# Performance work log

Hardware: AMD Instinct MI355X
Metric: run time of the kernel (lower is better)

Reference implementation:

```python
import jax, jax.numpy as jnp
import numpy as np
from jax import lax

B, T, N, C_IN = 1024, 10, 113, 4
E = N * 16
INV_STD = float(1.0 / np.sqrt(1.0 + 1e-5))  # eval-mode BatchNorm, running_mean=0, running_var=1
_DN = ('NHWC', 'HWIO', 'NHWC')  # (B,T,N,C) treated as NHWC, conv kernel (kt,1,Cin,Cout)


def _tconv(x, w, b):
    # x: (B,t,N,Cin), w: (3,1,Cin,Cout) -> (B,t-2,N,Cout); == Conv2d(Cin,Cout,(1,3)) in the torch layout
    return lax.conv_general_dilated(x, w, (1, 1), 'VALID', dimension_numbers=_DN) + b


def _gated_tcn(x, wp, bp, wq, bq, wr, br):
    # TemporalConv: relu(P * sigmoid(Q) + R)
    return jax.nn.relu(_tconv(x, wp, bp) * jax.nn.sigmoid(_tconv(x, wq, bq)) + _tconv(x, wr, br))


def _stconv(x, wp1, bp1, wq1, bq1, wr1, br1, cw, cb, wp2, bp2, wq2, bq2, wr2, br2, g, beta):
    h = _gated_tcn(x, wp1, bp1, wq1, bq1, wr1, br1)
    # ChebConv with K=1: only the identity term T_0 = x -> per-node linear (edge_index unused)
    h = jax.nn.relu(h @ cw + cb)
    h = _gated_tcn(h, wp2, bp2, wq2, bq2, wr2, br2)
    # BatchNorm2d over the node dim, eval mode (mean 0, var 1)
    return h * INV_STD * g[None, None, :, None] + beta[None, None, :, None]


def setup_inputs() -> dict:
    key = jax.random.key(0)
    ks = iter(jax.random.split(key, 48))

    def nrm(shape, s=0.1):
        return jax.random.normal(next(ks), shape, jnp.float32) * s

    d = {'x': nrm((B, T, N, C_IN), 1.0),
         'edge_index': jax.random.randint(next(ks), (2, E), 0, N)}
    # STConv block 1: in=4, hidden=32, out=64, kernel_size=3, K=1
    d['a_wp'] = nrm((3, 1, 4, 32)); d['a_bp'] = nrm((32,))
    d['a_wq'] = nrm((3, 1, 4, 32)); d['a_bq'] = nrm((32,))
    d['a_wr'] = nrm((3, 1, 4, 32)); d['a_br'] = nrm((32,))
    d['a_cw'] = nrm((32, 32));      d['a_cb'] = nrm((32,))
    d['a_wp2'] = nrm((3, 1, 32, 64)); d['a_bp2'] = nrm((64,))
    d['a_wq2'] = nrm((3, 1, 32, 64)); d['a_bq2'] = nrm((64,))
    d['a_wr2'] = nrm((3, 1, 32, 64)); d['a_br2'] = nrm((64,))
    d['a_g'] = jnp.ones((N,), jnp.float32); d['a_beta'] = jnp.zeros((N,), jnp.float32)
    # STConv block 2: in=64, hidden=32, out=16, kernel_size=3, K=1
    d['b_wp'] = nrm((3, 1, 64, 32)); d['b_bp'] = nrm((32,))
    d['b_wq'] = nrm((3, 1, 64, 32)); d['b_bq'] = nrm((32,))
    d['b_wr'] = nrm((3, 1, 64, 32)); d['b_br'] = nrm((32,))
    d['b_cw'] = nrm((32, 32));       d['b_cb'] = nrm((32,))
    d['b_wp2'] = nrm((3, 1, 32, 16)); d['b_bp2'] = nrm((16,))
    d['b_wq2'] = nrm((3, 1, 32, 16)); d['b_bq2'] = nrm((16,))
    d['b_wr2'] = nrm((3, 1, 32, 16)); d['b_br2'] = nrm((16,))
    d['b_g'] = jnp.ones((N,), jnp.float32); d['b_beta'] = jnp.zeros((N,), jnp.float32)
    # 113 per-node MLPs Linear(32,64)->ReLU->Linear(64,3), stacked as batched matmuls
    d['mlp_w1'] = nrm((N, 64, 32)); d['mlp_b1'] = nrm((N, 64))
    d['mlp_w2'] = nrm((N, 3, 64));  d['mlp_b2'] = nrm((N, 3))
    return d


def reference(x, edge_index, a_wp, a_bp, a_wq, a_bq, a_wr, a_br, a_cw, a_cb,
              a_wp2, a_bp2, a_wq2, a_bq2, a_wr2, a_br2, a_g, a_beta,
              b_wp, b_bp, b_wq, b_bq, b_wr, b_br, b_cw, b_cb,
              b_wp2, b_bp2, b_wq2, b_bq2, b_wr2, b_br2, b_g, b_beta,
              mlp_w1, mlp_b1, mlp_w2, mlp_b2):
    # dropout is identity in eval mode
    h = jax.nn.relu(_stconv(x, a_wp, a_bp, a_wq, a_bq, a_wr, a_br, a_cw, a_cb,
                            a_wp2, a_bp2, a_wq2, a_bq2, a_wr2, a_br2, a_g, a_beta))
    h = jax.nn.relu(_stconv(h, b_wp, b_bp, b_wq, b_bq, b_wr, b_br, b_cw, b_cb,
                            b_wp2, b_bp2, b_wq2, b_bq2, b_wr2, b_br2, b_g, b_beta))
    # h: (B, 2, N, 16); torch flatten(x[:,:,k,:], start_dim=1) interleaves (t, c) -> (B, N, 32)
    feat = jnp.transpose(h, (0, 2, 1, 3)).reshape(h.shape[0], N, 32)
    # all 113 tiny MLPs fused into two batched matmuls
    hid = jax.nn.relu(jnp.einsum('bnf,nhf->bnh', feat, mlp_w1) + mlp_b1)
    return jnp.einsum('bnh,noh->bno', hid, mlp_w2) + mlp_b2  # (B, 113, 3)
```

## Files before the change

### kernel.cpp

```cpp
#include <hip/hip_runtime.h>
#include <hip/hip_bf16.h>
#include <math.h>


namespace {

constexpr int NT = 512;
constexpr int NP = 32;
constexpr float INV_STD = 0.9999950000374997f;

typedef __attribute__((ext_vector_type(8))) short bf16x8;
typedef __attribute__((ext_vector_type(4))) float f32x4;

constexpr int OFF_CHEB_A = 0;
constexpr int OFF_CHEB_B = 1024;
constexpr int OFF_A2     = 2048;
constexpr int OFF_B1     = 20480;
constexpr int OFF_B2     = 38912;
constexpr int OFF_S1B    = 43520;
constexpr int OFF_W1     = 46592;
constexpr int OFF_W2     = 278016;

__device__ __forceinline__ unsigned short f2bf(float f){
  unsigned int u = __float_as_uint(f);
  u += 0x7fffu + ((u >> 16) & 1u);
  return (unsigned short)(u >> 16);
}
__device__ __forceinline__ unsigned short f2bf_fast(float f){
  return __bfloat16_as_ushort(__float2bfloat16(f));
}
__device__ __forceinline__ f32x4 bcast(float v){ f32x4 r; r[0]=v; r[1]=v; r[2]=v; r[3]=v; return r; }

struct Params {
  const float *x;
  const float *awp,*abp,*awq,*abq,*awr,*abr,*acw,*acb;
  const float *awp2,*abp2,*awq2,*abq2,*awr2,*abr2,*ag,*abeta;
  const float *bwp,*bbp,*bwq,*bbq,*bwr,*bbr,*bcw,*bcb;
  const float *bwp2,*bbp2,*bwq2,*bbq2,*bwr2,*bbr2,*bg,*bbeta;
  const float *w1,*b1,*w2,*b2;
  float *out;
};

__global__ void stgcn_prep(const Params p, unsigned short* __restrict__ W)
{
  int e = blockIdx.x*256 + threadIdx.x;
  if (e < 2048){
    const float* src = (e < 1024) ? p.acw : p.bcw;
    const int j = e & 1023, co = j >> 5, k = j & 31;
    W[e] = f2bf(src[k*32 + co]);
    return;
  }
  e -= 2048;
  if (e < 18432){
    const int mat = e / 6144, j = e % 6144, co = j / 96, k = j % 96;
    const float* src = mat==0 ? p.awp2 : (mat==1 ? p.awq2 : p.awr2);
    W[OFF_A2 + e] = f2bf(src[k*64 + co]);
    return;
  }
  e -= 18432;
  if (e < 18432){
    const int mat = e / 6144, j = e % 6144, co = j / 192, k = j % 192;
    const float* src = mat==0 ? p.bwp : (mat==1 ? p.bwq : p.bwr);
    W[OFF_B1 + e] = f2bf(src[k*32 + co]);
    return;
  }
  e -= 18432;
  if (e < 4608){
    const int mat = e / 1536, j = e % 1536, co = j / 96, k = j % 96;
    const float* src = mat==0 ? p.bwp2 : (mat==1 ? p.bwq2 : p.bwr2);
    W[OFF_B2 + e] = f2bf(src[k*16 + co]);
    return;
  }
  e -= 4608;
  if (e < 3072){
    const int mat = e / 1024, j = e % 1024, co = j >> 5, k = j & 31;
    const int tt = k >> 3, ci = k & 7;
    const float* src = mat==0 ? p.awp : (mat==1 ? p.awq : p.awr);
    W[OFF_S1B + e] = (ci < 4 && tt < 3) ? f2bf(src[(tt*4+ci)*32 + co])
                                        : (unsigned short)0;
    return;
  }
  e -= 3072;
  if (e < 231424){ W[OFF_W1 + e] = f2bf(p.w1[e]); return; }
  e -= 231424;
  if (e < 21696){ W[OFF_W2 + e] = f2bf(p.w2[e]); }
}

template<int TOUT, int CIN, int COUT, int NK, int RSTI, int PSTI, int RSTO, int PSTO,
         int KP, int EPI, int MJOBS, int MSTEP, bool RELOADB>
__device__ __forceinline__ void mfma_stage(const unsigned short* __restrict__ aB,
    const unsigned short* __restrict__ gW, unsigned short* __restrict__ oB,
    const float* __restrict__ gb0, const float* __restrict__ gb1,
    const float* __restrict__ gb2,
    const int Mtile0, const int Ntile, const int lm, const int lk,
    const float bnsc, const float bnbt)
{
  const unsigned short* wbase = gW + (Ntile*16 + lm)*KP + lk*8;
  const int colbase = Ntile*16 + lk*4;
  bf16x8 wp[NK], wq[NK], wr[NK];
  if constexpr (!RELOADB){
    #pragma unroll
    for (int ks = 0; ks < NK; ++ks){
      wp[ks] = *reinterpret_cast<const bf16x8*>(wbase + ks*32);
      if constexpr (EPI >= 1){
        wq[ks] = *reinterpret_cast<const bf16x8*>(wbase +   COUT*KP + ks*32);
        wr[ks] = *reinterpret_cast<const bf16x8*>(wbase + 2*COUT*KP + ks*32);
      }
    }
  }
  const f32x4 b0v = *reinterpret_cast<const f32x4*>(gb0 + colbase);
  f32x4 b1v, b2v;
  if constexpr (EPI >= 1){
    b1v = *reinterpret_cast<const f32x4*>(gb1 + colbase);
    b2v = *reinterpret_cast<const f32x4*>(gb2 + colbase);
  }

  #pragma unroll 1
  for (int j = 0; j < MJOBS; ++j){
    const int m  = (Mtile0 + j*MSTEP)*16 + lm;
    const int pr = m / TOUT;
    const int t  = m - pr*TOUT;
    f32x4 aP = b0v, aQ, aR;
    if constexpr (EPI >= 1){ aQ = b1v; aR = b2v; }
    #pragma unroll
    for (int ks = 0; ks < NK; ++ks){
      bf16x8 fp, fq, fr;
      if constexpr (RELOADB){
        fp = *reinterpret_cast<const bf16x8*>(wbase + ks*32);
        if constexpr (EPI >= 1){
          fq = *reinterpret_cast<const bf16x8*>(wbase +   COUT*KP + ks*32);
          fr = *reinterpret_cast<const bf16x8*>(wbase + 2*COUT*KP + ks*32);
        }
      } else {
        fp = wp[ks];
        if constexpr (EPI >= 1){ fq = wq[ks]; fr = wr[ks]; }
      }
      int elem;
      if constexpr (CIN == 32) elem = pr*PSTI + (t + ks)*RSTI + lk*8;
      else                     elem = pr*PSTI + (t + (ks>>1))*RSTI + (ks&1)*32 + lk*8;
      const bf16x8 a = *reinterpret_cast<const bf16x8*>(aB + elem);
      aP = __builtin_amdgcn_mfma_f32_16x16x32_bf16(fp, a, aP, 0, 0, 0);
      if constexpr (EPI >= 1){
        aQ = __builtin_amdgcn_mfma_f32_16x16x32_bf16(fq, a, aQ, 0, 0, 0);
        aR = __builtin_amdgcn_mfma_f32_16x16x32_bf16(fr, a, aR, 0, 0, 0);
      }
    }
    ushort4 pk;
    unsigned short pv[4];
    #pragma unroll
    for (int r = 0; r < 4; ++r){
      float v;
      if constexpr (EPI == 0) v = fmaxf(aP[r], 0.f);
      else {
        const float sig = 1.f/(1.f + __expf(-aQ[r]));
        v = fmaxf(fmaf(aP[r], sig, aR[r]), 0.f);
        if constexpr (EPI == 2) v = fmaxf(fmaf(v, bnsc, bnbt), 0.f);
      }
      pv[r] = f2bf_fast(v);
    }
    pk.x = pv[0]; pk.y = pv[1]; pk.z = pv[2]; pk.w = pv[3];
    *reinterpret_cast<ushort4*>(oB + pr*PSTO + t*RSTO + colbase) = pk;
  }
}

__device__ __forceinline__ void mfma_stage4(const unsigned short* __restrict__ aB,
    const unsigned short* __restrict__ gW, unsigned short* __restrict__ oB,
    const float* __restrict__ gb0, const float* __restrict__ gb1,
    const float* __restrict__ gb2,
    const int Mtile0, const int Ntile, const int lm, const int lk)
{
  const unsigned short* wbase = gW + (Ntile*16 + lm)*192 + lk*8;
  const int colbase = Ntile*16 + lk*4;
  f32x4 aP[2], aQ[2], aR[2];
  {
    const f32x4 b0v = *reinterpret_cast<const f32x4*>(gb0 + colbase);
    const f32x4 b1v = *reinterpret_cast<const f32x4*>(gb1 + colbase);
    const f32x4 b2v = *reinterpret_cast<const f32x4*>(gb2 + colbase);
    #pragma unroll
    for (int j=0;j<2;++j){ aP[j]=b0v; aQ[j]=b1v; aR[j]=b2v; }
  }
  #pragma unroll 1
  for (int kb = 0; kb < 2; ++kb){
    bf16x8 wp[3], wq[3], wr[3];
    #pragma unroll
    for (int s = 0; s < 3; ++s){
      const int ks = kb*3 + s;
      wp[s] = *reinterpret_cast<const bf16x8*>(wbase +         ks*32);
      wq[s] = *reinterpret_cast<const bf16x8*>(wbase +  6144 + ks*32);
      wr[s] = *reinterpret_cast<const bf16x8*>(wbase + 12288 + ks*32);
    }
    #pragma unroll
    for (int j = 0; j < 2; ++j){
      const int m  = (Mtile0 + j*4)*16 + lm;
      const int pr = m >> 2, t = m & 3;
      #pragma unroll
      for (int s = 0; s < 3; ++s){
        const int ks = kb*3 + s;
        const int elem = pr*432 + (t + (ks>>1))*72 + (ks&1)*32 + lk*8;
        const bf16x8 a = *reinterpret_cast<const bf16x8*>(aB + elem);
        aP[j] = __builtin_amdgcn_mfma_f32_16x16x32_bf16(wp[s], a, aP[j], 0,0,0);
        aQ[j] = __builtin_amdgcn_mfma_f32_16x16x32_bf16(wq[s], a, aQ[j], 0,0,0);
        aR[j] = __builtin_amdgcn_mfma_f32_16x16x32_bf16(wr[s], a, aR[j], 0,0,0);
      }
    }
  }
  #pragma unroll
  for (int j = 0; j < 2; ++j){
    const int m  = (Mtile0 + j*4)*16 + lm;
    const int pr = m >> 2, t = m & 3;
    ushort4 pk;
    unsigned short pv[4];
    #pragma unroll
    for (int r = 0; r < 4; ++r){
      const float sig = 1.f/(1.f + __expf(-aQ[j][r]));
      pv[r] = f2bf_fast(fmaxf(fmaf(aP[j][r], sig, aR[j][r]), 0.f));
    }
    pk.x = pv[0]; pk.y = pv[1]; pk.z = pv[2]; pk.w = pv[3];
    *reinterpret_cast<ushort4*>(oB + pr*160 + t*40 + colbase) = pk;
  }
}

__global__ __launch_bounds__(NT, 6) void stgcn_main(const Params p,
    const unsigned short* __restrict__ W)
{
  __shared__ __align__(16) unsigned short smem[24064];
  unsigned short* const bufA = smem;
  unsigned short* const bufB = smem + 13824;
  unsigned short* const sxb  = bufB;

  const int tid = threadIdx.x;
  const int l   = tid & 63;
  const int wid = tid >> 6;
  const int lm  = l & 15;
  const int lk  = l >> 4;
  const int n   = blockIdx.x >> 5;
  const int b0  = (blockIdx.x & 31) * NP;

  for (int i = tid; i < NP*22; i += NT){
    const int pr = i / 22, c = i - pr*22;
    const int t  = c >> 1;
    unsigned short v0=0,v1=0,v2=0,v3=0;
    if (!(c & 1) && t < 10){
      const float4 xf = *reinterpret_cast<const float4*>(
          &p.x[(size_t)(((b0+pr)*10 + t)*113 + n)*4]);
      v0 = f2bf(xf.x); v1 = f2bf(xf.y); v2 = f2bf(xf.z); v3 = f2bf(xf.w);
    }
    ushort4 pk; pk.x=v0; pk.y=v1; pk.z=v2; pk.w=v3;
    *reinterpret_cast<ushort4*>(&sxb[i*4]) = pk;
  }
  __syncthreads();

  mfma_stage<8,32,32,1, 8,88, 40,320, 32, 1, 4,4, false>(
      sxb, W+OFF_S1B, bufA, p.abp, p.abq, p.abr, wid>>1, wid&1, lm, lk, 0.f, 0.f);
  __syncthreads();

  mfma_stage<8,32,32,1, 40,320, 40,320, 32, 0, 4,4, false>(
      bufA, W+OFF_CHEB_A, bufB, p.acb, p.acb, p.acb, wid>>1, wid&1, lm, lk, 0.f, 0.f);
  __syncthreads();

  {
    const float bnsc = INV_STD * p.ag[n], bnbt = p.abeta[n];
    mfma_stage<6,32,64,3, 40,320, 72,432, 96, 2, 6,2, true>(
        bufB, W+OFF_A2, bufA, p.abp2, p.abq2, p.abr2, wid>>2, wid&3, lm, lk, bnsc, bnbt);
  }
  __syncthreads();

  mfma_stage4(bufA, W+OFF_B1, bufB, p.bbp, p.bbq, p.bbr, wid>>1, wid&1, lm, lk);
  __syncthreads();

  mfma_stage<4,32,32,1, 40,160, 40,160, 32, 0, 2,4, false>(
      bufB, W+OFF_CHEB_B, bufA, p.bcb, p.bcb, p.bcb, wid>>1, wid&1, lm, lk, 0.f, 0.f);
  __syncthreads();

  if (wid < 4){
    const float bnsc = INV_STD * p.bg[n], bnbt = p.bbeta[n];
    mfma_stage<2,32,16,3, 40,160, 16,40, 96, 2, 1,1, false>(
        bufA, W+OFF_B2, bufB, p.bbp2, p.bbq2, p.bbr2, wid, 0, lm, lk, bnsc, bnbt);
  }
  __syncthreads();

  mfma_stage<1,32,64,1, 16,40, 16,72, 32, 0, 1,1, false>(
      bufB, W+OFF_W1 + n*2048, bufA, p.b1 + n*64, p.b1, p.b1, wid&1, wid>>1, lm, lk, 0.f, 0.f);
  __syncthreads();

  if (wid < 2){
    const unsigned short* WM2 = W + OFF_W2 + n*192;
    const int Mtile = wid;
    const int m = Mtile*16 + lm;
    const int lmo = (lm < 3) ? lm : 0;
    f32x4 acc = bcast(0.f);
    if (lk == 0){ acc[0]=p.b2[n*3]; acc[1]=p.b2[n*3+1]; acc[2]=p.b2[n*3+2]; }
    #pragma unroll
    for (int ks = 0; ks < 2; ++ks){
      const bf16x8 aw = *reinterpret_cast<const bf16x8*>(WM2 + lmo*64 + ks*32 + lk*8);
      const bf16x8 bh = *reinterpret_cast<const bf16x8*>(bufA + m*72 + ks*32 + lk*8);
      acc = __builtin_amdgcn_mfma_f32_16x16x32_bf16(aw, bh, acc, 0, 0, 0);
    }
    if (lk == 0){
      float* op = p.out + (size_t)((b0 + m)*113 + n)*3;
      op[0] = acc[0]; op[1] = acc[1]; op[2] = acc[2];
    }
  }
}

}

extern "C" void kernel_launch(void* const* d_in, const int* in_sizes, int n_in,
                              void* d_out, int out_size, void* d_ws, size_t ws_size,
                              hipStream_t stream) {
  (void)in_sizes; (void)n_in; (void)ws_size; (void)out_size;
  Params p;
  p.x     = (const float*)d_in[0];
  p.awp   = (const float*)d_in[2];  p.abp   = (const float*)d_in[3];
  p.awq   = (const float*)d_in[4];  p.abq   = (const float*)d_in[5];
  p.awr   = (const float*)d_in[6];  p.abr   = (const float*)d_in[7];
  p.acw   = (const float*)d_in[8];  p.acb   = (const float*)d_in[9];
  p.awp2  = (const float*)d_in[10]; p.abp2  = (const float*)d_in[11];
  p.awq2  = (const float*)d_in[12]; p.abq2  = (const float*)d_in[13];
  p.awr2  = (const float*)d_in[14]; p.abr2  = (const float*)d_in[15];
  p.ag    = (const float*)d_in[16]; p.abeta = (const float*)d_in[17];
  p.bwp   = (const float*)d_in[18]; p.bbp   = (const float*)d_in[19];
  p.bwq   = (const float*)d_in[20]; p.bbq   = (const float*)d_in[21];
  p.bwr   = (const float*)d_in[22]; p.bbr   = (const float*)d_in[23];
  p.bcw   = (const float*)d_in[24]; p.bcb   = (const float*)d_in[25];
  p.bwp2  = (const float*)d_in[26]; p.bbp2  = (const float*)d_in[27];
  p.bwq2  = (const float*)d_in[28]; p.bbq2  = (const float*)d_in[29];
  p.bwr2  = (const float*)d_in[30]; p.bbr2  = (const float*)d_in[31];
  p.bg    = (const float*)d_in[32]; p.bbeta = (const float*)d_in[33];
  p.w1    = (const float*)d_in[34]; p.b1    = (const float*)d_in[35];
  p.w2    = (const float*)d_in[36]; p.b2    = (const float*)d_in[37];
  p.out   = (float*)d_out;

  unsigned short* W = (unsigned short*)d_ws;

  stgcn_prep<<<1171, 256, 0, stream>>>(p, W);

  const int tiles = 113 * 32;
  stgcn_main<<<tiles, NT, 0, stream>>>(p, W);
}
```

Measured before the change: 138.8 us.

## Switch several stages to 32x32x16 MFMA tiles with reworked wave mapping

Adds a 32x32x16 bf16 MFMA stage template and uses it for the first gated TCN, both Cheb linear layers and the second gated TCN of block one. Each wave now owns a full 32-row tile with 16-wide accumulators, and the A2 stage is split into 12 jobs over two rounds. The goal is fewer MFMA issues and fewer operand loads per output. In exchange each lane holds more accumulator registers, so launch bounds drop from 6 to 4 waves per SIMD, which may lower occupancy. The input conversion also switches to the fast bf16 rounding routine.

Result: slower. 201.2 us (+44.9%).

```diff
diff --git a/kernel.cpp b/kernel.cpp
--- a/kernel.cpp
+++ b/kernel.cpp
@@ -9,8 +9,9 @@
 constexpr int NP = 32;
 constexpr float INV_STD = 0.9999950000374997f;
 
-typedef __attribute__((ext_vector_type(8))) short bf16x8;
-typedef __attribute__((ext_vector_type(4))) float f32x4;
+typedef __attribute__((ext_vector_type(8)))  short bf16x8;
+typedef __attribute__((ext_vector_type(4)))  float f32x4;
+typedef __attribute__((ext_vector_type(16))) float f32x16;
 
 constexpr int OFF_CHEB_A = 0;
 constexpr int OFF_CHEB_B = 1024;
@@ -84,6 +85,81 @@
   if (e < 231424){ W[OFF_W1 + e] = f2bf(p.w1[e]); return; }
   e -= 231424;
   if (e < 21696){ W[OFF_W2 + e] = f2bf(p.w2[e]); }
+}
+
+template<int TOUT, int NK, int MODE, int RSTI, int PSTI, int RSTO, int PSTO,
+         int KP, int EPI, bool RELOAD, int COUT>
+__device__ __forceinline__ void mfma_stage32(
+    const unsigned short* __restrict__ aB,
+    const unsigned short* __restrict__ gW,
+    unsigned short* __restrict__ oB,
+    const float* __restrict__ gb0, const float* __restrict__ gb1,
+    const float* __restrict__ gb2,
+    const int Mtile, const int Ntile, const int lr, const int hi,
+    const float bnsc, const float bnbt)
+{
+  const unsigned short* wbase = gW + (Ntile*32 + lr)*KP + hi*8;
+  const int cb = Ntile*32 + hi*4;
+  f32x16 aP, aQ, aR;
+  #pragma unroll
+  for (int g = 0; g < 4; ++g){
+    const f32x4 b0 = *reinterpret_cast<const f32x4*>(gb0 + cb + g*8);
+    #pragma unroll
+    for (int r = 0; r < 4; ++r) aP[g*4+r] = b0[r];
+    if constexpr (EPI >= 1){
+      const f32x4 b1 = *reinterpret_cast<const f32x4*>(gb1 + cb + g*8);
+      const f32x4 b2 = *reinterpret_cast<const f32x4*>(gb2 + cb + g*8);
+      #pragma unroll
+      for (int r = 0; r < 4; ++r){ aQ[g*4+r] = b1[r]; aR[g*4+r] = b2[r]; }
+    }
+  }
+  const int m  = Mtile*32 + lr;
+  const int pr = m / TOUT;
+  const int t  = m - pr*TOUT;
+
+  auto kbody = [&](const int ks){
+    const bf16x8 fp = *reinterpret_cast<const bf16x8*>(wbase + ks*16);
+    bf16x8 fq, fr;
+    if constexpr (EPI >= 1){
+      fq = *reinterpret_cast<const bf16x8*>(wbase +   COUT*KP + ks*16);
+      fr = *reinterpret_cast<const bf16x8*>(wbase + 2*COUT*KP + ks*16);
+    }
+    int elem;
+    if constexpr (MODE == 0) elem = pr*PSTI + (t + 2*ks + hi)*RSTI;
+    else if constexpr (MODE == 1) elem = pr*PSTI + t*RSTI + ks*16 + hi*8;
+    else elem = pr*PSTI + (t + (ks>>1))*RSTI + (ks&1)*16 + hi*8;
+    const bf16x8 a = *reinterpret_cast<const bf16x8*>(aB + elem);
+    aP = __builtin_amdgcn_mfma_f32_32x32x16_bf16(fp, a, aP, 0, 0, 0);
+    if constexpr (EPI >= 1){
+      aQ = __builtin_amdgcn_mfma_f32_32x32x16_bf16(fq, a, aQ, 0, 0, 0);
+      aR = __builtin_amdgcn_mfma_f32_32x32x16_bf16(fr, a, aR, 0, 0, 0);
+    }
+  };
+  if constexpr (RELOAD){
+    #pragma unroll 1
+    for (int ks = 0; ks < NK; ++ks) kbody(ks);
+  } else {
+    #pragma unroll
+    for (int ks = 0; ks < NK; ++ks) kbody(ks);
+  }
+
+  #pragma unroll
+  for (int g = 0; g < 4; ++g){
+    unsigned short pv[4];
+    #pragma unroll
+    for (int r = 0; r < 4; ++r){
+      float v;
+      if constexpr (EPI == 0) v = fmaxf(aP[g*4+r], 0.f);
+      else {
+        const float sig = 1.f/(1.f + __expf(-aQ[g*4+r]));
+        v = fmaxf(fmaf(aP[g*4+r], sig, aR[g*4+r]), 0.f);
+        if constexpr (EPI == 2) v = fmaxf(fmaf(v, bnsc, bnbt), 0.f);
+      }
+      pv[r] = f2bf_fast(v);
+    }
+    ushort4 pk; pk.x=pv[0]; pk.y=pv[1]; pk.z=pv[2]; pk.w=pv[3];
+    *reinterpret_cast<ushort4*>(oB + pr*PSTO + t*RSTO + cb + g*8) = pk;
+  }
 }
 
 template<int TOUT, int CIN, int COUT, int NK, int RSTI, int PSTI, int RSTO, int PSTO,
@@ -220,7 +296,7 @@
   }
 }
 
-__global__ __launch_bounds__(NT, 6) void stgcn_main(const Params p,
+__global__ __launch_bounds__(NT, 4) void stgcn_main(const Params p,
     const unsigned short* __restrict__ W)
 {
   __shared__ __align__(16) unsigned short smem[24064];
@@ -233,6 +309,8 @@
   const int wid = tid >> 6;
   const int lm  = l & 15;
   const int lk  = l >> 4;
+  const int lr  = l & 31;
+  const int hi  = l >> 5;
   const int n   = blockIdx.x >> 5;
   const int b0  = (blockIdx.x & 31) * NP;
 
@@ -243,33 +321,41 @@
     if (!(c & 1) && t < 10){
       const float4 xf = *reinterpret_cast<const float4*>(
           &p.x[(size_t)(((b0+pr)*10 + t)*113 + n)*4]);
-      v0 = f2bf(xf.x); v1 = f2bf(xf.y); v2 = f2bf(xf.z); v3 = f2bf(xf.w);
+      v0 = f2bf_fast(xf.x); v1 = f2bf_fast(xf.y);
+      v2 = f2bf_fast(xf.z); v3 = f2bf_fast(xf.w);
     }
     ushort4 pk; pk.x=v0; pk.y=v1; pk.z=v2; pk.w=v3;
     *reinterpret_cast<ushort4*>(&sxb[i*4]) = pk;
   }
   __syncthreads();
 
-  mfma_stage<8,32,32,1, 8,88, 40,320, 32, 1, 4,4, false>(
-      sxb, W+OFF_S1B, bufA, p.abp, p.abq, p.abr, wid>>1, wid&1, lm, lk, 0.f, 0.f);
-  __syncthreads();
-
-  mfma_stage<8,32,32,1, 40,320, 40,320, 32, 0, 4,4, false>(
-      bufA, W+OFF_CHEB_A, bufB, p.acb, p.acb, p.acb, wid>>1, wid&1, lm, lk, 0.f, 0.f);
+  mfma_stage32<8, 2, 0, 8,88, 40,320, 32, 1, false, 32>(
+      sxb, W+OFF_S1B, bufA, p.abp, p.abq, p.abr, wid, 0, lr, hi, 0.f, 0.f);
+  __syncthreads();
+
+  mfma_stage32<8, 2, 1, 40,320, 40,320, 32, 0, false, 32>(
+      bufA, W+OFF_CHEB_A, bufB, p.acb, p.acb, p.acb, wid, 0, lr, hi, 0.f, 0.f);
   __syncthreads();
 
   {
     const float bnsc = INV_STD * p.ag[n], bnbt = p.abeta[n];
-    mfma_stage<6,32,64,3, 40,320, 72,432, 96, 2, 6,2, true>(
-        bufB, W+OFF_A2, bufA, p.abp2, p.abq2, p.abr2, wid>>2, wid&3, lm, lk, bnsc, bnbt);
+    #pragma unroll 1
+    for (int rep = 0; rep < 2; ++rep){
+      const int j = wid + rep*8;
+      if (j < 12)
+        mfma_stage32<6, 6, 2, 40,320, 72,432, 96, 2, true, 64>(
+            bufB, W+OFF_A2, bufA, p.abp2, p.abq2, p.abr2, j>>1, j&1, lr, hi, bnsc, bnbt);
+    }
   }
   __syncthreads();
 
   mfma_stage4(bufA, W+OFF_B1, bufB, p.bbp, p.bbq, p.bbr, wid>>1, wid&1, lm, lk);
   __syncthreads();
 
-  mfma_stage<4,32,32,1, 40,160, 40,160, 32, 0, 2,4, false>(
-      bufB, W+OFF_CHEB_B, bufA, p.bcb, p.bcb, p.bcb, wid>>1, wid&1, lm, lk, 0.f, 0.f);
+  if (wid < 4){
+    mfma_stage32<4, 2, 1, 40,160, 40,160, 32, 0, false, 32>(
+        bufB, W+OFF_CHEB_B, bufA, p.bcb, p.bcb, p.bcb, wid, 0, lr, hi, 0.f, 0.f);
+  }
   __syncthreads();
 
   if (wid < 4){
```

## Split fused STGCN kernel into five staged kernels via global workspace

Applied to the files above, without the earlier changes.

Replaces the single per-node fused kernel, which kept every intermediate in shared memory, with five kernels that write bf16 intermediates (H1C, H2, H3, H3C) to the workspace. Each kernel maps waves directly to 16-row MFMA tiles over a flat (node, batch, time) index, with fewer barriers and loads that go straight to registers. The old kernel is kept as a fallback when the workspace is too small. The trade is extra global memory traffic, tens of MB of intermediates, plus extra launch overhead, in exchange for simpler per-stage kernels with better occupancy and parallelism.

Result: slower. 291.8 us (+110.2%).

```diff
diff --git a/kernel.cpp b/kernel.cpp
--- a/kernel.cpp
+++ b/kernel.cpp
@@ -5,8 +5,6 @@
 
 namespace {
 
-constexpr int NT = 512;
-constexpr int NP = 32;
 constexpr float INV_STD = 0.9999950000374997f;
 
 typedef __attribute__((ext_vector_type(8))) short bf16x8;
@@ -20,6 +18,10 @@
 constexpr int OFF_S1B    = 43520;
 constexpr int OFF_W1     = 46592;
 constexpr int OFF_W2     = 278016;
+constexpr size_t E_A   = 524288;
+constexpr size_t E_H3C = 524288 + 14811136;
+constexpr size_t E_H2  = 524288 + 29622272;
+constexpr size_t NEED_BYTES = 149159936;
 
 __device__ __forceinline__ unsigned short f2bf(float f){
   unsigned int u = __float_as_uint(f);
@@ -86,6 +88,319 @@
   if (e < 21696){ W[OFF_W2 + e] = f2bf(p.w2[e]); }
 }
 
+
+__global__ __launch_bounds__(512, 4) void k1_front(const Params p,
+    const unsigned short* __restrict__ W, unsigned short* __restrict__ H1C)
+{
+  __shared__ unsigned short h1L[8192];
+  const int tid = threadIdx.x, l = tid & 63, wid = tid >> 6;
+  const int lm = l & 15, lk = l >> 4;
+  unsigned short* hl = h1L + wid*1024;
+  const int Mt0 = (blockIdx.x*8 + wid) * 2;
+
+  bf16x8 av[2];
+  #pragma unroll
+  for (int mt = 0; mt < 2; ++mt){
+    const int m = (Mt0+mt)*16 + lm;
+    const int pair = m >> 3, t = m & 7;
+    const int nn = pair >> 10, b = pair & 1023;
+    bf16x8 a;
+    #pragma unroll
+    for (int j = 0; j < 8; ++j) a[j] = 0;
+    if (lk < 3){
+      const float4 xf = *reinterpret_cast<const float4*>(
+          &p.x[(size_t)((b*10 + t + lk)*113 + nn)*4]);
+      a[0]=(short)f2bf(xf.x); a[1]=(short)f2bf(xf.y);
+      a[2]=(short)f2bf(xf.z); a[3]=(short)f2bf(xf.w);
+    }
+    av[mt] = a;
+  }
+  #pragma unroll
+  for (int Nt = 0; Nt < 2; ++Nt){
+    const unsigned short* wb = W + OFF_S1B + (Nt*16+lm)*32 + lk*8;
+    const bf16x8 wp = *reinterpret_cast<const bf16x8*>(wb);
+    const bf16x8 wq = *reinterpret_cast<const bf16x8*>(wb + 1024);
+    const bf16x8 wr = *reinterpret_cast<const bf16x8*>(wb + 2048);
+    const int cb = Nt*16 + lk*4;
+    const f32x4 b0 = *reinterpret_cast<const f32x4*>(p.abp + cb);
+    const f32x4 b1 = *reinterpret_cast<const f32x4*>(p.abq + cb);
+    const f32x4 b2 = *reinterpret_cast<const f32x4*>(p.abr + cb);
+    #pragma unroll
+    for (int mt = 0; mt < 2; ++mt){
+      f32x4 aP = b0, aQ = b1, aR = b2;
+      aP = __builtin_amdgcn_mfma_f32_16x16x32_bf16(wp, av[mt], aP, 0,0,0);
+      aQ = __builtin_amdgcn_mfma_f32_16x16x32_bf16(wq, av[mt], aQ, 0,0,0);
+      aR = __builtin_amdgcn_mfma_f32_16x16x32_bf16(wr, av[mt], aR, 0,0,0);
+      unsigned short pv[4];
+      #pragma unroll
+      for (int r = 0; r < 4; ++r){
+        const float sig = 1.f/(1.f + __expf(-aQ[r]));
+        pv[r] = f2bf_fast(fmaxf(fmaf(aP[r], sig, aR[r]), 0.f));
+      }
+      ushort4 pk; pk.x=pv[0]; pk.y=pv[1]; pk.z=pv[2]; pk.w=pv[3];
+      *reinterpret_cast<ushort4*>(hl + (mt*16+lm)*32 + cb) = pk;
+    }
+  }
+  bf16x8 bv[2];
+  #pragma unroll
+  for (int mt = 0; mt < 2; ++mt)
+    bv[mt] = *reinterpret_cast<const bf16x8*>(hl + (mt*16+lm)*32 + lk*8);
+  #pragma unroll
+  for (int Nt = 0; Nt < 2; ++Nt){
+    const bf16x8 wc = *reinterpret_cast<const bf16x8*>(
+        W + OFF_CHEB_A + (Nt*16+lm)*32 + lk*8);
+    const int cb = Nt*16 + lk*4;
+    const f32x4 b0 = *reinterpret_cast<const f32x4*>(p.acb + cb);
+    #pragma unroll
+    for (int mt = 0; mt < 2; ++mt){
+      f32x4 acc = b0;
+      acc = __builtin_amdgcn_mfma_f32_16x16x32_bf16(wc, bv[mt], acc, 0,0,0);
+      const int m = (Mt0+mt)*16 + lm;
+      const int pair = m >> 3, t = m & 7;
+      unsigned short pv[4];
+      #pragma unroll
+      for (int r = 0; r < 4; ++r) pv[r] = f2bf_fast(fmaxf(acc[r], 0.f));
+      ushort4 pk; pk.x=pv[0]; pk.y=pv[1]; pk.z=pv[2]; pk.w=pv[3];
+      *reinterpret_cast<ushort4*>(H1C + (size_t)pair*256 + t*32 + cb) = pk;
+    }
+  }
+}
+
+__global__ __launch_bounds__(512, 4) void k2_s3(const Params p,
+    const unsigned short* __restrict__ W, const unsigned short* __restrict__ H1C,
+    unsigned short* __restrict__ H2)
+{
+  const int tid = threadIdx.x, l = tid & 63, wid = tid >> 6;
+  const int lm = l & 15, lk = l >> 4;
+  const int Mt0 = (blockIdx.x*8 + wid) * 2;
+
+  bf16x8 av[2][3];
+  int prs[2], ts[2];
+  #pragma unroll
+  for (int mt = 0; mt < 2; ++mt){
+    const int m = (Mt0+mt)*16 + lm;
+    const int pair = m / 6, t = m - pair*6;
+    prs[mt] = pair; ts[mt] = t;
+    const unsigned short* ab = H1C + (size_t)pair*256 + t*32 + lk*8;
+    #pragma unroll
+    for (int ks = 0; ks < 3; ++ks)
+      av[mt][ks] = *reinterpret_cast<const bf16x8*>(ab + ks*32);
+  }
+  #pragma unroll
+  for (int Nt = 0; Nt < 4; ++Nt){
+    const unsigned short* wb = W + OFF_A2 + (Nt*16+lm)*96 + lk*8;
+    bf16x8 wp[3], wq[3], wr[3];
+    #pragma unroll
+    for (int ks = 0; ks < 3; ++ks){
+      wp[ks] = *reinterpret_cast<const bf16x8*>(wb + ks*32);
+      wq[ks] = *reinterpret_cast<const bf16x8*>(wb +  6144 + ks*32);
+      wr[ks] = *reinterpret_cast<const bf16x8*>(wb + 12288 + ks*32);
+    }
+    const int cb = Nt*16 + lk*4;
+    const f32x4 b0 = *reinterpret_cast<const f32x4*>(p.abp2 + cb);
+    const f32x4 b1 = *reinterpret_cast<const f32x4*>(p.abq2 + cb);
+    const f32x4 b2 = *reinterpret_cast<const f32x4*>(p.abr2 + cb);
+    #pragma unroll
+    for (int mt = 0; mt < 2; ++mt){
+      f32x4 aP = b0, aQ = b1, aR = b2;
+      #pragma unroll
+      for (int ks = 0; ks < 3; ++ks){
+        aP = __builtin_amdgcn_mfma_f32_16x16x32_bf16(wp[ks], av[mt][ks], aP, 0,0,0);
+        aQ = __builtin_amdgcn_mfma_f32_16x16x32_bf16(wq[ks], av[mt][ks], aQ, 0,0,0);
+        aR = __builtin_amdgcn_mfma_f32_16x16x32_bf16(wr[ks], av[mt][ks], aR, 0,0,0);
+      }
+      const int pair = prs[mt], nn = pair >> 10;
+      const float bns = INV_STD * p.ag[nn], bnb = p.abeta[nn];
+      unsigned short pv[4];
+      #pragma unroll
+      for (int r = 0; r < 4; ++r){
+        const float sig = 1.f/(1.f + __expf(-aQ[r]));
+        float v = fmaxf(fmaf(aP[r], sig, aR[r]), 0.f);
+        v = fmaxf(fmaf(v, bns, bnb), 0.f);
+        pv[r] = f2bf_fast(v);
+      }
+      ushort4 pk; pk.x=pv[0]; pk.y=pv[1]; pk.z=pv[2]; pk.w=pv[3];
+      *reinterpret_cast<ushort4*>(H2 + (size_t)pair*384 + ts[mt]*64 + cb) = pk;
+    }
+  }
+}
+
+__global__ __launch_bounds__(512, 4) void k3_s4(const Params p,
+    const unsigned short* __restrict__ W, const unsigned short* __restrict__ H2,
+    unsigned short* __restrict__ H3)
+{
+  const int tid = threadIdx.x, l = tid & 63, wid = tid >> 6;
+  const int lm = l & 15, lk = l >> 4;
+  const int Mt = blockIdx.x*8 + wid;
+  const int m = Mt*16 + lm;
+  const int pair = m >> 2, t = m & 3;
+
+  bf16x8 av[6];
+  {
+    const unsigned short* ab = H2 + (size_t)pair*384 + lk*8;
+    #pragma unroll
+    for (int ks = 0; ks < 6; ++ks)
+      av[ks] = *reinterpret_cast<const bf16x8*>(ab + (t + (ks>>1))*64 + (ks&1)*32);
+  }
+  #pragma unroll
+  for (int Nt = 0; Nt < 2; ++Nt){
+    const unsigned short* wb = W + OFF_B1 + (Nt*16+lm)*192 + lk*8;
+    const int cb = Nt*16 + lk*4;
+    f32x4 aP = *reinterpret_cast<const f32x4*>(p.bbp + cb);
+    f32x4 aQ = *reinterpret_cast<const f32x4*>(p.bbq + cb);
+    f32x4 aR = *reinterpret_cast<const f32x4*>(p.bbr + cb);
+    #pragma unroll
+    for (int kb = 0; kb < 2; ++kb){
+      bf16x8 wp[3], wq[3], wr[3];
+      #pragma unroll
+      for (int s = 0; s < 3; ++s){
+        const int ks = kb*3 + s;
+        wp[s] = *reinterpret_cast<const bf16x8*>(wb +         ks*32);
+        wq[s] = *reinterpret_cast<const bf16x8*>(wb +  6144 + ks*32);
+        wr[s] = *reinterpret_cast<const bf16x8*>(wb + 12288 + ks*32);
+      }
+      #pragma unroll
+      for (int s = 0; s < 3; ++s){
+        const int ks = kb*3 + s;
+        aP = __builtin_amdgcn_mfma_f32_16x16x32_bf16(wp[s], av[ks], aP, 0,0,0);
+        aQ = __builtin_amdgcn_mfma_f32_16x16x32_bf16(wq[s], av[ks], aQ, 0,0,0);
+        aR = __builtin_amdgcn_mfma_f32_16x16x32_bf16(wr[s], av[ks], aR, 0,0,0);
+      }
+    }
+    unsigned short pv[4];
+    #pragma unroll
+    for (int r = 0; r < 4; ++r){
+      const float sig = 1.f/(1.f + __expf(-aQ[r]));
+      pv[r] = f2bf_fast(fmaxf(fmaf(aP[r], sig, aR[r]), 0.f));
+    }
+    ushort4 pk; pk.x=pv[0]; pk.y=pv[1]; pk.z=pv[2]; pk.w=pv[3];
+    *reinterpret_cast<ushort4*>(H3 + (size_t)pair*128 + t*32 + cb) = pk;
+  }
+}
+
+__global__ __launch_bounds__(512, 4) void k4_cheb2(const Params p,
+    const unsigned short* __restrict__ W, const unsigned short* __restrict__ H3,
+    unsigned short* __restrict__ H3C)
+{
+  const int tid = threadIdx.x, l = tid & 63, wid = tid >> 6;
+  const int lm = l & 15, lk = l >> 4;
+  const int Mt0 = (blockIdx.x*8 + wid) * 4;
+
+  bf16x8 av[4];
+  int prs[4], ts[4];
+  #pragma unroll
+  for (int mt = 0; mt < 4; ++mt){
+    const int m = (Mt0+mt)*16 + lm;
+    const int pair = m >> 2, t = m & 3;
+    prs[mt] = pair; ts[mt] = t;
+    av[mt] = *reinterpret_cast<const bf16x8*>(H3 + (size_t)pair*128 + t*32 + lk*8);
+  }
+  #pragma unroll
+  for (int Nt = 0; Nt < 2; ++Nt){
+    const bf16x8 wc = *reinterpret_cast<const bf16x8*>(
+        W + OFF_CHEB_B + (Nt*16+lm)*32 + lk*8);
+    const int cb = Nt*16 + lk*4;
+    const f32x4 b0 = *reinterpret_cast<const f32x4*>(p.bcb + cb);
+    #pragma unroll
+    for (int mt = 0; mt < 4; ++mt){
+      f32x4 acc = b0;
+      acc = __builtin_amdgcn_mfma_f32_16x16x32_bf16(wc, av[mt], acc, 0,0,0);
+      unsigned short pv[4];
+      #pragma unroll
+      for (int r = 0; r < 4; ++r) pv[r] = f2bf_fast(fmaxf(acc[r], 0.f));
+      ushort4 pk; pk.x=pv[0]; pk.y=pv[1]; pk.z=pv[2]; pk.w=pv[3];
+      *reinterpret_cast<ushort4*>(H3C + (size_t)prs[mt]*128 + ts[mt]*32 + cb) = pk;
+    }
+  }
+}
+
+__global__ __launch_bounds__(512, 4) void k5_tail(const Params p,
+    const unsigned short* __restrict__ W, const unsigned short* __restrict__ H3C)
+{
+  __shared__ unsigned short sc[13312];
+  const int tid = threadIdx.x, l = tid & 63, wid = tid >> 6;
+  const int lm = l & 15, lk = l >> 4;
+  const int P0 = (blockIdx.x*8 + wid) * 16;
+  const int nn = P0 >> 10;
+  unsigned short* h4L  = sc + wid*1664;
+  unsigned short* hidL = h4L + 512;
+
+  {
+    const unsigned short* wb = W + OFF_B2 + lm*96 + lk*8;
+    bf16x8 wp[3], wq[3], wr[3];
+    #pragma unroll
+    for (int ks = 0; ks < 3; ++ks){
+      wp[ks] = *reinterpret_cast<const bf16x8*>(wb +        ks*32);
+      wq[ks] = *reinterpret_cast<const bf16x8*>(wb + 1536 + ks*32);
+      wr[ks] = *reinterpret_cast<const bf16x8*>(wb + 3072 + ks*32);
+    }
+    const int cb = lk*4;
+    const f32x4 b0 = *reinterpret_cast<const f32x4*>(p.bbp2 + cb);
+    const f32x4 b1 = *reinterpret_cast<const f32x4*>(p.bbq2 + cb);
+    const f32x4 b2 = *reinterpret_cast<const f32x4*>(p.bbr2 + cb);
+    const float bns = INV_STD * p.bg[nn], bnb = p.bbeta[nn];
+    #pragma unroll
+    for (int mt = 0; mt < 2; ++mt){
+      const int ml = mt*16 + lm;
+      const int pl = ml >> 1, t = ml & 1;
+      const unsigned short* ab = H3C + (size_t)(P0 + pl)*128 + t*32 + lk*8;
+      f32x4 aP = b0, aQ = b1, aR = b2;
+      #pragma unroll
+      for (int ks = 0; ks < 3; ++ks){
+        const bf16x8 a = *reinterpret_cast<const bf16x8*>(ab + ks*32);
+        aP = __builtin_amdgcn_mfma_f32_16x16x32_bf16(wp[ks], a, aP, 0,0,0);
+        aQ = __builtin_amdgcn_mfma_f32_16x16x32_bf16(wq[ks], a, aQ, 0,0,0);
+        aR = __builtin_amdgcn_mfma_f32_16x16x32_bf16(wr[ks], a, aR, 0,0,0);
+      }
+      unsigned short pv[4];
+      #pragma unroll
+      for (int r = 0; r < 4; ++r){
+        const float sig = 1.f/(1.f + __expf(-aQ[r]));
+        float v = fmaxf(fmaf(aP[r], sig, aR[r]), 0.f);
+        v = fmaxf(fmaf(v, bns, bnb), 0.f);
+        pv[r] = f2bf_fast(v);
+      }
+      ushort4 pk; pk.x=pv[0]; pk.y=pv[1]; pk.z=pv[2]; pk.w=pv[3];
+      *reinterpret_cast<ushort4*>(h4L + pl*32 + t*16 + cb) = pk;
+    }
+  }
+  {
+    const bf16x8 bh = *reinterpret_cast<const bf16x8*>(h4L + lm*32 + lk*8);
+    #pragma unroll
+    for (int Nt = 0; Nt < 4; ++Nt){
+      const bf16x8 wf = *reinterpret_cast<const bf16x8*>(
+          W + OFF_W1 + nn*2048 + (Nt*16+lm)*32 + lk*8);
+      const int cb = Nt*16 + lk*4;
+      f32x4 acc = *reinterpret_cast<const f32x4*>(p.b1 + nn*64 + cb);
+      acc = __builtin_amdgcn_mfma_f32_16x16x32_bf16(wf, bh, acc, 0,0,0);
+      unsigned short pv[4];
+      #pragma unroll
+      for (int r = 0; r < 4; ++r) pv[r] = f2bf_fast(fmaxf(acc[r], 0.f));
+      ushort4 pk; pk.x=pv[0]; pk.y=pv[1]; pk.z=pv[2]; pk.w=pv[3];
+      *reinterpret_cast<ushort4*>(hidL + lm*72 + cb) = pk;
+    }
+  }
+  {
+    const unsigned short* WM2 = W + OFF_W2 + nn*192;
+    const int lmo = (lm < 3) ? lm : 0;
+    f32x4 acc = bcast(0.f);
+    if (lk == 0){ acc[0]=p.b2[nn*3]; acc[1]=p.b2[nn*3+1]; acc[2]=p.b2[nn*3+2]; }
+    #pragma unroll
+    for (int ks = 0; ks < 2; ++ks){
+      const bf16x8 aw = *reinterpret_cast<const bf16x8*>(WM2 + lmo*64 + ks*32 + lk*8);
+      const bf16x8 bh = *reinterpret_cast<const bf16x8*>(hidL + lm*72 + ks*32 + lk*8);
+      acc = __builtin_amdgcn_mfma_f32_16x16x32_bf16(aw, bh, acc, 0,0,0);
+    }
+    if (lk == 0){
+      const int pair = P0 + lm;
+      const int b = pair & 1023;
+      float* op = p.out + ((size_t)b*113 + nn)*3;
+      op[0] = acc[0]; op[1] = acc[1]; op[2] = acc[2];
+    }
+  }
+}
+
+
 template<int TOUT, int CIN, int COUT, int NK, int RSTI, int PSTI, int RSTO, int PSTO,
          int KP, int EPI, int MJOBS, int MSTEP, bool RELOADB>
 __device__ __forceinline__ void mfma_stage(const unsigned short* __restrict__ aB,
@@ -114,7 +429,6 @@
     b1v = *reinterpret_cast<const f32x4*>(gb1 + colbase);
     b2v = *reinterpret_cast<const f32x4*>(gb2 + colbase);
   }
-
   #pragma unroll 1
   for (int j = 0; j < MJOBS; ++j){
     const int m  = (Mtile0 + j*MSTEP)*16 + lm;
@@ -220,7 +534,7 @@
   }
 }
 
-__global__ __launch_bounds__(NT, 6) void stgcn_main(const Params p,
+__global__ __launch_bounds__(512, 4) void stgcn_main(const Params p,
     const unsigned short* __restrict__ W)
 {
   __shared__ __align__(16) unsigned short smem[24064];
@@ -234,9 +548,9 @@
   const int lm  = l & 15;
   const int lk  = l >> 4;
   const int n   = blockIdx.x >> 5;
-  const int b0  = (blockIdx.x & 31) * NP;
-
-  for (int i = tid; i < NP*22; i += NT){
+  const int b0  = (blockIdx.x & 31) * 32;
+
+  for (int i = tid; i < 32*22; i += 512){
     const int pr = i / 22, c = i - pr*22;
     const int t  = c >> 1;
     unsigned short v0=0,v1=0,v2=0,v3=0;
@@ -253,40 +567,32 @@
   mfma_stage<8,32,32,1, 8,88, 40,320, 32, 1, 4,4, false>(
       sxb, W+OFF_S1B, bufA, p.abp, p.abq, p.abr, wid>>1, wid&1, lm, lk, 0.f, 0.f);
   __syncthreads();
-
   mfma_stage<8,32,32,1, 40,320, 40,320, 32, 0, 4,4, false>(
       bufA, W+OFF_CHEB_A, bufB, p.acb, p.acb, p.acb, wid>>1, wid&1, lm, lk, 0.f, 0.f);
   __syncthreads();
-
   {
     const float bnsc = INV_STD * p.ag[n], bnbt = p.abeta[n];
     mfma_stage<6,32,64,3, 40,320, 72,432, 96, 2, 6,2, true>(
         bufB, W+OFF_A2, bufA, p.abp2, p.abq2, p.abr2, wid>>2, wid&3, lm, lk, bnsc, bnbt);
   }
   __syncthreads();
-
   mfma_stage4(bufA, W+OFF_B1, bufB, p.bbp, p.bbq, p.bbr, wid>>1, wid&1, lm, lk);
   __syncthreads();
-
   mfma_stage<4,32,32,1, 40,160, 40,160, 32, 0, 2,4, false>(
       bufB, W+OFF_CHEB_B, bufA, p.bcb, p.bcb, p.bcb, wid>>1, wid&1, lm, lk, 0.f, 0.f);
   __syncthreads();
-
   if (wid < 4){
     const float bnsc = INV_STD * p.bg[n], bnbt = p.bbeta[n];
     mfma_stage<2,32,16,3, 40,160, 16,40, 96, 2, 1,1, false>(
         bufA, W+OFF_B2, bufB, p.bbp2, p.bbq2, p.bbr2, wid, 0, lm, lk, bnsc, bnbt);
   }
   __syncthreads();
-
   mfma_stage<1,32,64,1, 16,40, 16,72, 32, 0, 1,1, false>(
       bufB, W+OFF_W1 + n*2048, bufA, p.b1 + n*64, p.b1, p.b1, wid&1, wid>>1, lm, lk, 0.f, 0.f);
   __syncthreads();
-
   if (wid < 2){
     const unsigned short* WM2 = W + OFF_W2 + n*192;
-    const int Mtile = wid;
-    const int m = Mtile*16 + lm;
+    const int m = wid*16 + lm;
     const int lmo = (lm < 3) ? lm : 0;
     f32x4 acc = bcast(0.f);
     if (lk == 0){ acc[0]=p.b2[n*3]; acc[1]=p.b2[n*3+1]; acc[2]=p.b2[n*3+2]; }
@@ -308,7 +614,7 @@
 extern "C" void kernel_launch(void* const* d_in, const int* in_sizes, int n_in,
                               void* d_out, int out_size, void* d_ws, size_t ws_size,
                               hipStream_t stream) {
-  (void)in_sizes; (void)n_in; (void)ws_size; (void)out_size;
+  (void)in_sizes; (void)n_in; (void)out_size;
   Params p;
   p.x     = (const float*)d_in[0];
   p.awp   = (const float*)d_in[2];  p.abp   = (const float*)d_in[3];
@@ -335,6 +641,17 @@
 
   stgcn_prep<<<1171, 256, 0, stream>>>(p, W);
 
-  const int tiles = 113 * 32;
-  stgcn_main<<<tiles, NT, 0, stream>>>(p, W);
-}
+  if (ws_size >= NEED_BYTES){
+    unsigned short* H1C = W + E_A;
+    unsigned short* H2  = W + E_H2;
+    unsigned short* H3  = W + E_A;
+    unsigned short* H3C = W + E_H3C;
+    k1_front<<<3616, 512, 0, stream>>>(p, W, H1C);
+    k2_s3   <<<2712, 512, 0, stream>>>(p, W, H1C, H2);
+    k3_s4   <<<3616, 512, 0, stream>>>(p, W, H2, H3);
+    k4_cheb2<<< 904, 512, 0, stream>>>(p, W, H3, H3C);
+    k5_tail <<< 904, 512, 0, stream>>>(p, W, H3C);
+  } else {
+    stgcn_main<<<113*32, 512, 0, stream>>>(p, W);
+  }
+}
```
